# Optimization experiments

Hardware: AMD Instinct MI355X
Metric: run time of the kernel (lower is better)

Reference implementation:

```python
import jax, jax.numpy as jnp
import numpy as np

VOCAB = 50000
EMB = 300
HID = 1024
MAXLEN = 128
BATCH = 256
M2 = 512


def _xavier(k, shape):
    lim = np.sqrt(6.0 / (shape[0] + shape[-1]))
    return jax.random.uniform(k, shape, jnp.float32, -lim, lim)


def setup_inputs() -> dict:
    key = jax.random.key(0)
    ks = jax.random.split(key, 16)
    return {
        "input1": jax.random.randint(ks[0], (BATCH, MAXLEN), 0, VOCAB, dtype=jnp.int32),
        "input2": jax.random.randint(ks[1], (BATCH, MAXLEN), 0, VOCAB, dtype=jnp.int32),
        "seqlen1": jax.random.randint(ks[2], (BATCH,), 1, MAXLEN + 1, dtype=jnp.int32),
        "seqlen2": jax.random.randint(ks[3], (BATCH,), 1, MAXLEN + 1, dtype=jnp.int32),
        "embeddings": jax.random.normal(ks[4], (VOCAB, EMB), jnp.float32) * 0.1,
        "lstm_kernel": _xavier(ks[5], (EMB + HID, 4 * HID)),
        "lstm_bias": jnp.zeros((4 * HID,), jnp.float32),
        "c1_init": _xavier(ks[6], (BATCH, HID)),
        "h1_init": _xavier(ks[7], (BATCH, HID)),
        "c2_init": _xavier(ks[8], (BATCH, HID)),
        "h2_init": _xavier(ks[9], (BATCH, HID)),
        "W_h": _xavier(ks[10], (HID + 1, HID + 1)),
        "W1": _xavier(ks[11], (3 * (HID + 1) + 1 + BATCH, M2)),
        "b1": _xavier(ks[12], (1, M2)),
        "W2": _xavier(ks[13], (M2, 2)),
        "b2": _xavier(ks[14], (1, 2)),
    }


def _lstm_last_state(x, seqlen, c0, h0, kernel, bias):
    # TF BasicLSTMCell: gates in order i, j, f, o; forget_bias=1.0.
    # dynamic_rnn(sequence_length=...) freezes state past each row's seqlen.
    E = x.shape[-1]
    Wx, Wh = kernel[:E], kernel[E:]
    xg = jnp.einsum('bte,eg->btg', x, Wx) + bias  # [B,T,4H], input proj hoisted out of scan
    T = x.shape[1]

    def step(carry, inputs):
        c, h = carry
        xg_t, t = inputs
        g = xg_t + h @ Wh
        i, j, f, o = jnp.split(g, 4, axis=-1)
        c_new = jax.nn.sigmoid(f + 1.0) * c + jax.nn.sigmoid(i) * jnp.tanh(j)
        h_new = jnp.tanh(c_new) * jax.nn.sigmoid(o)
        valid = (t < seqlen)[:, None]
        return (jnp.where(valid, c_new, c), jnp.where(valid, h_new, h)), None

    (c, h), _ = jax.lax.scan(step, (c0, h0), (jnp.swapaxes(xg, 0, 1), jnp.arange(T)))
    return h


def reference(input1, input2, seqlen1, seqlen2, embeddings, lstm_kernel, lstm_bias,
              c1_init, h1_init, c2_init, h2_init, W_h, W1, b1, W2, b2):
    x1 = embeddings[input1]  # [B,T,E]
    x2 = embeddings[input2]
    h1 = _lstm_last_state(x1, seqlen1, c1_init, h1_init, lstm_kernel, lstm_bias)
    h2 = _lstm_last_state(x2, seqlen2, c2_init, h2_init, lstm_kernel, lstm_bias)
    len1 = (seqlen1.astype(jnp.float32) / float(MAXLEN))[:, None]
    len2 = (seqlen2.astype(jnp.float32) / float(MAXLEN))[:, None]
    h1 = jnp.concatenate([h1, len1], axis=1)  # [B,H+1]
    h2 = jnp.concatenate([h2, len2], axis=1)
    h_dist = jnp.sum(jnp.square(h1 - h2), axis=1, keepdims=True)  # [B,1]
    h_mul = h1 * h2                                               # [B,H+1]
    h_interaction = (h1 @ W_h) @ h2.T                             # [B,B] bilinear block
    h_combined = jnp.concatenate([h1, h2, h_dist, h_mul, h_interaction], axis=1)
    e1 = jax.nn.relu(h_combined @ W1 + b1)  # dropout keep_prob=1 at inference -> identity
    return e1 @ W2 + b2  # [B,2] logits
```

## Files before the change

kernel.cpp:

```cpp
#include <hip/hip_runtime.h>
#include <hip/hip_bf16.h>

typedef __bf16 bf16;
typedef __bf16 bf16x8 __attribute__((ext_vector_type(8)));
typedef float f32x4 __attribute__((ext_vector_type(4)));

#define N_ROWS   512
#define HID      1024
#define KX       320
#define KTOT     1344
#define NSTEPS   128
#define EMB_D    300
#define HC_W     3332

#define WBT_OFF   0UL
#define XB_OFF    11010048UL
#define HB_OFF    52953088UL
#define BIASP_OFF 55050240UL
#define CB_OFF    55066624UL
#define HC_OFF    11010048UL
#define H2T_OFF   14422016UL
#define T1_OFF    15471616UL
#define E1_OFF    16521216UL


__device__ __forceinline__ float sigm(float x) { return 1.f / (1.f + __expf(-x)); }
__device__ __forceinline__ float tanh_fast(float x) {
  float xc = fminf(fmaxf(x, -15.f), 15.f);
  float e = __expf(2.f * xc);
  return (e - 1.f) / (e + 1.f);
}

__device__ __forceinline__ void lds_barrier() {
  asm volatile("s_waitcnt lgkmcnt(0)" ::: "memory");
  __builtin_amdgcn_sched_barrier(0);
  __builtin_amdgcn_s_barrier();
  __builtin_amdgcn_sched_barrier(0);
}

__global__ void pack_wbt(const float* __restrict__ lk, bf16* __restrict__ wbt) {
  int p = blockIdx.x * 256 + threadIdx.x;
  int k = blockIdx.y;
  int cb = p >> 6, g = (p >> 4) & 3, c = p & 15;
  int oc = g * HID + cb * 16 + c;
  float v = 0.f;
  if (k < KX) { if (k < EMB_D) v = lk[(size_t)k * 4096 + oc]; }
  else v = lk[(size_t)(EMB_D + k - KX) * 4096 + oc];
  wbt[(size_t)p * KTOT + k] = (bf16)v;
}

__global__ void pack_xb(const int* __restrict__ in1, const int* __restrict__ in2,
                        const float* __restrict__ emb, bf16* __restrict__ xb) {
  int r = blockIdx.x;
  int t = blockIdx.y * 8 + threadIdx.x / 40;
  int e8 = threadIdx.x % 40;
  int tok = (r < 256) ? in1[r * 128 + t] : in2[(r - 256) * 128 + t];
  const float* er = emb + (size_t)tok * EMB_D + e8 * 8;
  bf16x8 v;
  if (e8 < 37) {
#pragma unroll
    for (int i = 0; i < 8; ++i) v[i] = (bf16)er[i];
  } else {
#pragma unroll
    for (int i = 0; i < 8; ++i) {
      int e = e8 * 8 + i;
      v[i] = (e < EMB_D) ? (bf16)er[i] : (bf16)0.f;
    }
  }
  *reinterpret_cast<bf16x8*>(&xb[((size_t)t * N_ROWS + r) * KX + e8 * 8]) = v;
}

__global__ void pack_misc(const float* __restrict__ h1i, const float* __restrict__ h2i,
                          const float* __restrict__ c1i, const float* __restrict__ c2i,
                          const float* __restrict__ bias, bf16* __restrict__ hb0,
                          float* __restrict__ biasp, float* __restrict__ Cb) {
  int idx = blockIdx.x * 256 + threadIdx.x;
  if (idx < N_ROWS * HID) {
    int r = idx >> 10, k = idx & 1023;
    float v = (r < 256) ? h1i[(size_t)r * HID + k] : h2i[(size_t)(r - 256) * HID + k];
    hb0[idx] = (bf16)v;
    float cv = (r < 256) ? c1i[(size_t)r * HID + k] : c2i[(size_t)(r - 256) * HID + k];
    Cb[idx] = cv;
  }
  if (idx < 4096) {
    int cb = idx >> 6, g = (idx >> 4) & 3, c = idx & 15;
    biasp[idx] = bias[g * HID + cb * 16 + c];
  }
}

__launch_bounds__(256, 2)
__global__ void lstm_step(const bf16* __restrict__ xb, const bf16* __restrict__ wbt,
                          bf16* __restrict__ hb, const float* __restrict__ biasp,
                          float* __restrict__ Cb, const int* __restrict__ s1,
                          const int* __restrict__ s2, int t) {
  __shared__ bf16 As[2][128][64];
  __shared__ bf16 Bs[2][64][64];
  const int tid = threadIdx.x;
  const int wave = tid >> 6;
  const int lane = tid & 63;
  const int lrow = lane & 15;
  const int hi = lane >> 4;
  const int l7 = lane & 7;
  const int bid = blockIdx.x;
  const int rb = bid >> 6;
  const int cb = bid & 63;
  const int r0 = rb * 128;

  const int cellabs = cb * 16 + lrow;

  int slen[2][4];
#pragma unroll
  for (int mi = 0; mi < 2; ++mi)
#pragma unroll
    for (int q = 0; q < 4; ++q) {
      int rr = r0 + wave * 32 + mi * 16 + hi * 4 + q;
      slen[mi][q] = (rr < 256) ? s1[rr] : s2[rr - 256];
    }

  float creg[2][4];
#pragma unroll
  for (int mi = 0; mi < 2; ++mi)
#pragma unroll
    for (int q = 0; q < 4; ++q) {
      int rr = r0 + wave * 32 + mi * 16 + hi * 4 + q;
      creg[mi][q] = Cb[(size_t)rr * HID + cellabs];
    }

  float bv[4];
#pragma unroll
  for (int ni = 0; ni < 4; ++ni)
    bv[ni] = biasp[cb * 64 + ni * 16 + lrow];

  const int a_r = tid >> 1, a_cb = (tid & 1) * 4;
  const int b_r = tid >> 2, b_cb = (tid & 3) * 2;

  const bf16* xt = xb + (size_t)t * N_ROWS * KX;
  const bf16* hc0 = hb + ((size_t)(t & 1) << 19);

  bf16x8 ra[4], rbv2[2];
  auto issue_loads = [&](int nkc) {
    const bf16* asrc = (nkc < 5)
        ? (xt + (size_t)(r0 + a_r) * KX + nkc * 64 + a_cb * 8)
        : (hc0 + ((size_t)(r0 + a_r) << 10) + (nkc * 64 - KX) + a_cb * 8);
#pragma unroll
    for (int q = 0; q < 4; ++q)
      ra[q] = *reinterpret_cast<const bf16x8*>(asrc + q * 8);
    const bf16* bsrc = wbt + (size_t)(cb * 64 + b_r) * KTOT + nkc * 64 + b_cb * 8;
#pragma unroll
    for (int q = 0; q < 2; ++q)
      rbv2[q] = *reinterpret_cast<const bf16x8*>(bsrc + q * 8);
  };
  auto stage_to = [&](int buf) {
#pragma unroll
    for (int q = 0; q < 4; ++q)
      *reinterpret_cast<bf16x8*>(&As[buf][a_r][((a_cb + q) ^ (a_r & 7)) << 3]) = ra[q];
#pragma unroll
    for (int q = 0; q < 2; ++q)
      *reinterpret_cast<bf16x8*>(&Bs[buf][b_r][((b_cb + q) ^ (b_r & 7)) << 3]) = rbv2[q];
  };

  issue_loads(0);
  stage_to(0);
  issue_loads(1);
  __syncthreads();
  int db = 0;

  f32x4 acc[2][4];
#pragma unroll
  for (int mi = 0; mi < 2; ++mi)
#pragma unroll
    for (int ni = 0; ni < 4; ++ni)
      acc[mi][ni] = f32x4{bv[ni], bv[ni], bv[ni], bv[ni]};

  for (int kc = 0; kc < 21; ++kc) {
    if (kc < 20) stage_to(db ^ 1);
    {
      int nkc = kc + 2;
      if (nkc <= 20) issue_loads(nkc);
    }
#pragma unroll
    for (int ks = 0; ks < 2; ++ks) {
      const int cs = (((ks << 2) | hi) ^ l7) << 3;
      bf16x8 af[2], bfv[4];
#pragma unroll
      for (int mi = 0; mi < 2; ++mi)
        af[mi] = *reinterpret_cast<const bf16x8*>(
            &As[db][wave * 32 + mi * 16 + lrow][cs]);
#pragma unroll
      for (int ni = 0; ni < 4; ++ni)
        bfv[ni] = *reinterpret_cast<const bf16x8*>(&Bs[db][ni * 16 + lrow][cs]);
#pragma unroll
      for (int mi = 0; mi < 2; ++mi)
#pragma unroll
        for (int ni = 0; ni < 4; ++ni)
          acc[mi][ni] = __builtin_amdgcn_mfma_f32_16x16x32_bf16(
              af[mi], bfv[ni], acc[mi][ni], 0, 0, 0);
    }
    lds_barrier();
    db ^= 1;
  }

  {
    const bf16* hc = hc0;
    bf16* hnb = hb + (((size_t)(t & 1) << 19) ^ ((size_t)1 << 19));
#pragma unroll
    for (int mi = 0; mi < 2; ++mi)
#pragma unroll
      for (int q = 0; q < 4; ++q) {
        float ig = acc[mi][0][q];
        float jg = acc[mi][1][q];
        float fg = acc[mi][2][q];
        float og = acc[mi][3][q];
        float cn = sigm(fg + 1.f) * creg[mi][q] + sigm(ig) * tanh_fast(jg);
        float hv = tanh_fast(cn) * sigm(og);
        int rr = r0 + wave * 32 + mi * 16 + hi * 4 + q;
        size_t off = ((size_t)rr << 10) + cellabs;
        float ho;
        if (t < slen[mi][q]) {
          Cb[off] = cn;
          ho = hv;
        } else {
          ho = (float)hc[off];
        }
        hnb[off] = (bf16)ho;
      }
  }
}

__global__ void feat_kernel(const bf16* __restrict__ hb0, const int* __restrict__ s1,
                            const int* __restrict__ s2, float* __restrict__ HC,
                            float* __restrict__ H2T) {
  int a = blockIdx.x;
  int tid = threadIdx.x;
  __shared__ float red[256];
  const bf16* h1r = hb0 + (size_t)a * HID;
  const bf16* h2r = hb0 + (size_t)(a + 256) * HID;
  float l1 = (float)s1[a] * (1.f / 128.f);
  float l2 = (float)s2[a] * (1.f / 128.f);
  float dacc = 0.f;
  for (int k = tid; k < 1025; k += 256) {
    float v1 = (k < HID) ? (float)h1r[k] : l1;
    float v2 = (k < HID) ? (float)h2r[k] : l2;
    HC[(size_t)a * HC_W + k] = v1;
    HC[(size_t)a * HC_W + 1025 + k] = v2;
    HC[(size_t)a * HC_W + 2051 + k] = v1 * v2;
    H2T[(size_t)k * 256 + a] = v2;
    float d = v1 - v2;
    dacc += d * d;
  }
  red[tid] = dacc;
  __syncthreads();
  for (int s = 128; s > 0; s >>= 1) {
    if (tid < s) red[tid] += red[tid + s];
    __syncthreads();
  }
  if (tid == 0) HC[(size_t)a * HC_W + 2050] = red[0];
}

__global__ void t1_kernel(const float* __restrict__ HC, const float* __restrict__ Wh,
                          float* __restrict__ T1) {
  int j = blockIdx.x * 256 + threadIdx.x;
  int a0 = blockIdx.y * 2;
  __shared__ float sh[2][1025];
  for (int idx = threadIdx.x; idx < 2050; idx += 256) {
    int r = (idx >= 1025) ? 1 : 0;
    int k = idx - r * 1025;
    sh[r][k] = HC[(size_t)(a0 + r) * HC_W + k];
  }
  __syncthreads();
  if (j < 1025) {
    float acc0 = 0.f, acc1 = 0.f;
    for (int k = 0; k < 1025; ++k) {
      float w = Wh[(size_t)k * 1025 + j];
      acc0 += sh[0][k] * w;
      acc1 += sh[1][k] * w;
    }
    T1[(size_t)a0 * 1025 + j] = acc0;
    T1[(size_t)(a0 + 1) * 1025 + j] = acc1;
  }
}

__global__ void inter_kernel(const float* __restrict__ T1, const float* __restrict__ H2T,
                             float* __restrict__ HC) {
  int a0 = blockIdx.x * 2;
  int b = threadIdx.x;
  __shared__ float sT[2][1025];
  for (int idx = threadIdx.x; idx < 2050; idx += 256) {
    int r = (idx >= 1025) ? 1 : 0;
    int k = idx - r * 1025;
    sT[r][k] = T1[(size_t)(a0 + r) * 1025 + k];
  }
  __syncthreads();
  float acc0 = 0.f, acc1 = 0.f;
  for (int k = 0; k < 1025; ++k) {
    float v = H2T[(size_t)k * 256 + b];
    acc0 += sT[0][k] * v;
    acc1 += sT[1][k] * v;
  }
  HC[(size_t)a0 * HC_W + 3076 + b] = acc0;
  HC[(size_t)(a0 + 1) * HC_W + 3076 + b] = acc1;
}

__global__ void e1_kernel(const float* __restrict__ HC, const float* __restrict__ W1,
                          const float* __restrict__ b1, float* __restrict__ E1) {
  int a0 = blockIdx.x * 2;
  int j = blockIdx.y * 256 + threadIdx.x;
  __shared__ float sh[2][HC_W];
  for (int idx = threadIdx.x; idx < 2 * HC_W; idx += 256) {
    int r = (idx >= HC_W) ? 1 : 0;
    int k = idx - r * HC_W;
    sh[r][k] = HC[(size_t)(a0 + r) * HC_W + k];
  }
  __syncthreads();
  float acc0 = 0.f, acc1 = 0.f;
  for (int k = 0; k < HC_W; ++k) {
    float w = W1[(size_t)k * 512 + j];
    acc0 += sh[0][k] * w;
    acc1 += sh[1][k] * w;
  }
  float bj = b1[j];
  E1[(size_t)a0 * 512 + j] = fmaxf(acc0 + bj, 0.f);
  E1[(size_t)(a0 + 1) * 512 + j] = fmaxf(acc1 + bj, 0.f);
}

__global__ void out_kernel(const float* __restrict__ E1, const float* __restrict__ W2,
                           const float* __restrict__ b2, float* __restrict__ out) {
  int a = blockIdx.x;
  int tid = threadIdx.x;
  __shared__ float red0[256], red1[256];
  float v0 = E1[(size_t)a * 512 + tid];
  float v1 = E1[(size_t)a * 512 + 256 + tid];
  float a0 = v0 * W2[2 * tid] + v1 * W2[2 * (tid + 256)];
  float a1 = v0 * W2[2 * tid + 1] + v1 * W2[2 * (tid + 256) + 1];
  red0[tid] = a0;
  red1[tid] = a1;
  __syncthreads();
  for (int s = 128; s > 0; s >>= 1) {
    if (tid < s) { red0[tid] += red0[tid + s]; red1[tid] += red1[tid + s]; }
    __syncthreads();
  }
  if (tid == 0) {
    out[2 * a] = red0[0] + b2[0];
    out[2 * a + 1] = red1[0] + b2[1];
  }
}

extern "C" void kernel_launch(void* const* d_in, const int* in_sizes, int n_in,
                              void* d_out, int out_size, void* d_ws, size_t ws_size,
                              hipStream_t stream) {
  const int*   input1 = (const int*)d_in[0];
  const int*   input2 = (const int*)d_in[1];
  const int*   seql1  = (const int*)d_in[2];
  const int*   seql2  = (const int*)d_in[3];
  const float* emb    = (const float*)d_in[4];
  const float* lk     = (const float*)d_in[5];
  const float* lbias  = (const float*)d_in[6];
  const float* c1i    = (const float*)d_in[7];
  const float* h1i    = (const float*)d_in[8];
  const float* c2i    = (const float*)d_in[9];
  const float* h2i    = (const float*)d_in[10];
  const float* W_h    = (const float*)d_in[11];
  const float* W1     = (const float*)d_in[12];
  const float* b1     = (const float*)d_in[13];
  const float* W2     = (const float*)d_in[14];
  const float* b2     = (const float*)d_in[15];

  char* ws = (char*)d_ws;
  bf16*     WbT   = (bf16*)(ws + WBT_OFF);
  bf16*     Xb    = (bf16*)(ws + XB_OFF);
  bf16*     Hb    = (bf16*)(ws + HB_OFF);
  float*    biasp = (float*)(ws + BIASP_OFF);
  float*    Cb    = (float*)(ws + CB_OFF);
  float*    HC    = (float*)(ws + HC_OFF);
  float*    H2T   = (float*)(ws + H2T_OFF);
  float*    T1    = (float*)(ws + T1_OFF);
  float*    E1    = (float*)(ws + E1_OFF);

  pack_wbt<<<dim3(16, 1344), 256, 0, stream>>>(lk, WbT);
  pack_xb<<<dim3(512, 16), 320, 0, stream>>>(input1, input2, emb, Xb);
  pack_misc<<<2048, 256, 0, stream>>>(h1i, h2i, c1i, c2i, lbias, Hb, biasp, Cb);

  for (int t = 0; t < NSTEPS; ++t)
    lstm_step<<<256, 256, 0, stream>>>(Xb, WbT, Hb, biasp, Cb, seql1, seql2, t);

  feat_kernel<<<256, 256, 0, stream>>>(Hb, seql1, seql2, HC, H2T);
  t1_kernel<<<dim3(5, 128), 256, 0, stream>>>(HC, W_h, T1);
  inter_kernel<<<128, 256, 0, stream>>>(T1, H2T, HC);
  e1_kernel<<<dim3(128, 2), 256, 0, stream>>>(HC, W1, b1, E1);
  out_kernel<<<256, 256, 0, stream>>>(E1, W2, b2, (float*)d_out);
}
```

Baseline: 2.458 ms.

## Tile weight pack through LDS and split-K the head matmuls for more blocks

pack_wbt now stages 64x64 tiles in shared memory, so reads from the fp32 LSTM kernel are float4-coalesced and writes to the packed bf16 weights are 16-byte vectors, replacing strided per-element accesses. The t1 and e1 head matmuls are split across two K halves (blockIdx.z) that write partial outputs to separate buffers. The consumer kernels add the halves, and bias plus ReLU move into out_kernel. inter_kernel now uses one row per block, doubling its grid. This adds workspace buffers and an extra partial-sum read, in exchange for more parallel blocks in the underfilled tail kernels.

```diff
diff --git a/kernel.cpp b/kernel.cpp
--- a/kernel.cpp
+++ b/kernel.cpp
@@ -20,8 +20,10 @@
 #define CB_OFF    55066624UL
 #define HC_OFF    11010048UL
 #define H2T_OFF   14422016UL
-#define T1_OFF    15471616UL
-#define E1_OFF    16521216UL
+#define T1A_OFF   15471616UL
+#define T1B_OFF   16521216UL
+#define E1A_OFF   17570816UL
+#define E1B_OFF   18095104UL
 
 
 __device__ __forceinline__ float sigm(float x) { return 1.f / (1.f + __expf(-x)); }
@@ -39,14 +41,38 @@
 }
 
 __global__ void pack_wbt(const float* __restrict__ lk, bf16* __restrict__ wbt) {
-  int p = blockIdx.x * 256 + threadIdx.x;
-  int k = blockIdx.y;
-  int cb = p >> 6, g = (p >> 4) & 3, c = p & 15;
-  int oc = g * HID + cb * 16 + c;
-  float v = 0.f;
-  if (k < KX) { if (k < EMB_D) v = lk[(size_t)k * 4096 + oc]; }
-  else v = lk[(size_t)(EMB_D + k - KX) * 4096 + oc];
-  wbt[(size_t)p * KTOT + k] = (bf16)v;
+  __shared__ float sh[64][65];
+  const int px = blockIdx.x;
+  const int k0 = blockIdx.y * 64;
+  const int t = threadIdx.x;
+  {
+    const int kk = t >> 2, g = t & 3;
+    const int k = k0 + kk;
+    const bool valid = (k < KX) ? (k < EMB_D) : true;
+    const int src = (k < KX) ? k : (k - 20);
+    const float* base = lk + (size_t)src * 4096 + g * 1024 + px * 16;
+#pragma unroll
+    for (int c4 = 0; c4 < 4; ++c4) {
+      float4 v = valid ? *reinterpret_cast<const float4*>(base + c4 * 4)
+                       : float4{0.f, 0.f, 0.f, 0.f};
+      sh[kk][g * 16 + c4 * 4 + 0] = v.x;
+      sh[kk][g * 16 + c4 * 4 + 1] = v.y;
+      sh[kk][g * 16 + c4 * 4 + 2] = v.z;
+      sh[kk][g * 16 + c4 * 4 + 3] = v.w;
+    }
+  }
+  __syncthreads();
+  {
+    const int pl = t >> 2, kq = (t & 3) * 16;
+    bf16 ov[16];
+#pragma unroll
+    for (int j = 0; j < 16; ++j) ov[j] = (bf16)sh[kq + j][pl];
+    bf16* dst = wbt + (size_t)(px * 64 + pl) * KTOT + k0 + kq;
+#pragma unroll
+    for (int j = 0; j < 2; ++j)
+      *reinterpret_cast<bf16x8*>(dst + j * 8) =
+          *reinterpret_cast<const bf16x8*>(&ov[j * 8]);
+  }
 }
 
 __global__ void pack_xb(const int* __restrict__ in1, const int* __restrict__ in2,
@@ -258,78 +284,80 @@
 }
 
 __global__ void t1_kernel(const float* __restrict__ HC, const float* __restrict__ Wh,
-                          float* __restrict__ T1) {
+                          float* __restrict__ T1a, float* __restrict__ T1b) {
   int j = blockIdx.x * 256 + threadIdx.x;
   int a0 = blockIdx.y * 2;
-  __shared__ float sh[2][1025];
-  for (int idx = threadIdx.x; idx < 2050; idx += 256) {
-    int r = (idx >= 1025) ? 1 : 0;
-    int k = idx - r * 1025;
-    sh[r][k] = HC[(size_t)(a0 + r) * HC_W + k];
+  int z = blockIdx.z;
+  const int k0 = z ? 513 : 0;
+  const int kn = z ? 512 : 513;
+  __shared__ float sh[2][513];
+  for (int idx = threadIdx.x; idx < 2 * kn; idx += 256) {
+    int r = (idx >= kn) ? 1 : 0;
+    int k = idx - r * kn;
+    sh[r][k] = HC[(size_t)(a0 + r) * HC_W + k0 + k];
   }
   __syncthreads();
   if (j < 1025) {
     float acc0 = 0.f, acc1 = 0.f;
-    for (int k = 0; k < 1025; ++k) {
-      float w = Wh[(size_t)k * 1025 + j];
+    for (int k = 0; k < kn; ++k) {
+      float w = Wh[(size_t)(k0 + k) * 1025 + j];
       acc0 += sh[0][k] * w;
       acc1 += sh[1][k] * w;
     }
+    float* T1 = z ? T1b : T1a;
     T1[(size_t)a0 * 1025 + j] = acc0;
     T1[(size_t)(a0 + 1) * 1025 + j] = acc1;
   }
 }
 
-__global__ void inter_kernel(const float* __restrict__ T1, const float* __restrict__ H2T,
-                             float* __restrict__ HC) {
-  int a0 = blockIdx.x * 2;
+__global__ void inter_kernel(const float* __restrict__ T1a, const float* __restrict__ T1b,
+                             const float* __restrict__ H2T, float* __restrict__ HC) {
+  int a = blockIdx.x;
   int b = threadIdx.x;
-  __shared__ float sT[2][1025];
-  for (int idx = threadIdx.x; idx < 2050; idx += 256) {
-    int r = (idx >= 1025) ? 1 : 0;
-    int k = idx - r * 1025;
-    sT[r][k] = T1[(size_t)(a0 + r) * 1025 + k];
-  }
-  __syncthreads();
-  float acc0 = 0.f, acc1 = 0.f;
-  for (int k = 0; k < 1025; ++k) {
-    float v = H2T[(size_t)k * 256 + b];
-    acc0 += sT[0][k] * v;
-    acc1 += sT[1][k] * v;
-  }
-  HC[(size_t)a0 * HC_W + 3076 + b] = acc0;
-  HC[(size_t)(a0 + 1) * HC_W + 3076 + b] = acc1;
+  __shared__ float sT[1025];
+  for (int k = threadIdx.x; k < 1025; k += 256)
+    sT[k] = T1a[(size_t)a * 1025 + k] + T1b[(size_t)a * 1025 + k];
+  __syncthreads();
+  float acc = 0.f;
+  for (int k = 0; k < 1025; ++k)
+    acc += sT[k] * H2T[(size_t)k * 256 + b];
+  HC[(size_t)a * HC_W + 3076 + b] = acc;
 }
 
 __global__ void e1_kernel(const float* __restrict__ HC, const float* __restrict__ W1,
-                          const float* __restrict__ b1, float* __restrict__ E1) {
+                          float* __restrict__ E1a, float* __restrict__ E1b) {
   int a0 = blockIdx.x * 2;
   int j = blockIdx.y * 256 + threadIdx.x;
-  __shared__ float sh[2][HC_W];
-  for (int idx = threadIdx.x; idx < 2 * HC_W; idx += 256) {
-    int r = (idx >= HC_W) ? 1 : 0;
-    int k = idx - r * HC_W;
-    sh[r][k] = HC[(size_t)(a0 + r) * HC_W + k];
+  int z = blockIdx.z;
+  const int k0 = z * 1666;
+  __shared__ float sh[2][1666];
+  for (int idx = threadIdx.x; idx < 2 * 1666; idx += 256) {
+    int r = (idx >= 1666) ? 1 : 0;
+    int k = idx - r * 1666;
+    sh[r][k] = HC[(size_t)(a0 + r) * HC_W + k0 + k];
   }
   __syncthreads();
   float acc0 = 0.f, acc1 = 0.f;
-  for (int k = 0; k < HC_W; ++k) {
-    float w = W1[(size_t)k * 512 + j];
+  for (int k = 0; k < 1666; ++k) {
+    float w = W1[(size_t)(k0 + k) * 512 + j];
     acc0 += sh[0][k] * w;
     acc1 += sh[1][k] * w;
   }
-  float bj = b1[j];
-  E1[(size_t)a0 * 512 + j] = fmaxf(acc0 + bj, 0.f);
-  E1[(size_t)(a0 + 1) * 512 + j] = fmaxf(acc1 + bj, 0.f);
-}
-
-__global__ void out_kernel(const float* __restrict__ E1, const float* __restrict__ W2,
+  float* E1 = z ? E1b : E1a;
+  E1[(size_t)a0 * 512 + j] = acc0;
+  E1[(size_t)(a0 + 1) * 512 + j] = acc1;
+}
+
+__global__ void out_kernel(const float* __restrict__ E1a, const float* __restrict__ E1b,
+                           const float* __restrict__ b1, const float* __restrict__ W2,
                            const float* __restrict__ b2, float* __restrict__ out) {
   int a = blockIdx.x;
   int tid = threadIdx.x;
   __shared__ float red0[256], red1[256];
-  float v0 = E1[(size_t)a * 512 + tid];
-  float v1 = E1[(size_t)a * 512 + 256 + tid];
+  size_t i0 = (size_t)a * 512 + tid;
+  size_t i1 = i0 + 256;
+  float v0 = fmaxf(E1a[i0] + E1b[i0] + b1[tid], 0.f);
+  float v1 = fmaxf(E1a[i1] + E1b[i1] + b1[tid + 256], 0.f);
   float a0 = v0 * W2[2 * tid] + v1 * W2[2 * (tid + 256)];
   float a1 = v0 * W2[2 * tid + 1] + v1 * W2[2 * (tid + 256) + 1];
   red0[tid] = a0;
@@ -373,10 +401,12 @@
   float*    Cb    = (float*)(ws + CB_OFF);
   float*    HC    = (float*)(ws + HC_OFF);
   float*    H2T   = (float*)(ws + H2T_OFF);
-  float*    T1    = (float*)(ws + T1_OFF);
-  float*    E1    = (float*)(ws + E1_OFF);
-
-  pack_wbt<<<dim3(16, 1344), 256, 0, stream>>>(lk, WbT);
+  float*    T1a   = (float*)(ws + T1A_OFF);
+  float*    T1b   = (float*)(ws + T1B_OFF);
+  float*    E1a   = (float*)(ws + E1A_OFF);
+  float*    E1b   = (float*)(ws + E1B_OFF);
+
+  pack_wbt<<<dim3(64, 21), 256, 0, stream>>>(lk, WbT);
   pack_xb<<<dim3(512, 16), 320, 0, stream>>>(input1, input2, emb, Xb);
   pack_misc<<<2048, 256, 0, stream>>>(h1i, h2i, c1i, c2i, lbias, Hb, biasp, Cb);
 
@@ -384,8 +414,8 @@
     lstm_step<<<256, 256, 0, stream>>>(Xb, WbT, Hb, biasp, Cb, seql1, seql2, t);
 
   feat_kernel<<<256, 256, 0, stream>>>(Hb, seql1, seql2, HC, H2T);
-  t1_kernel<<<dim3(5, 128), 256, 0, stream>>>(HC, W_h, T1);
-  inter_kernel<<<128, 256, 0, stream>>>(T1, H2T, HC);
-  e1_kernel<<<dim3(128, 2), 256, 0, stream>>>(HC, W1, b1, E1);
-  out_kernel<<<256, 256, 0, stream>>>(E1, W2, b2, (float*)d_out);
-}
+  t1_kernel<<<dim3(5, 128, 2), 256, 0, stream>>>(HC, W_h, T1a, T1b);
+  inter_kernel<<<256, 256, 0, stream>>>(T1a, T1b, H2T, HC);
+  e1_kernel<<<dim3(128, 2, 2), 256, 0, stream>>>(HC, W1, E1a, E1b);
+  out_kernel<<<256, 256, 0, stream>>>(E1a, E1b, b1, W2, b2, (float*)d_out);
+}
```

New measurement: 2.386 ms. 1.03x faster.
